# Kernel optimization log

Measured on AMD Instinct MI355X. Metric: run time of the kernel, lower is better.

Reference implementation:

```python
import jax, jax.numpy as jnp
import numpy as np

N_NODES = 100000
N_EDGES = 3200000
N_FEAT = 128
N_HID = 64


def gcn_conv(x, src, dst, ew, W, b, n):
    # x: [N, Fin]; src/dst: [E'] incl. self-loops; ew: [E'] edge weights
    xw = x @ W  # [N, Fout]
    deg = jax.ops.segment_sum(ew, dst, num_segments=n)  # [N]
    dinv = jnp.where(deg > 0, jax.lax.rsqrt(jnp.maximum(deg, 1e-12)), 0.0)
    norm = dinv[src] * ew * dinv[dst]  # [E']
    out = jax.ops.segment_sum(norm[:, None] * xw[src], dst, num_segments=n)
    return out + b


def setup_inputs() -> dict:
    key = jax.random.key(0)
    k = jax.random.split(key, 8)
    x = jax.random.normal(k[0], (N_NODES, N_FEAT), dtype=jnp.float32)
    edge_index = jax.random.randint(k[1], (2, N_EDGES), 0, N_NODES, dtype=jnp.int32)
    edge_attr = jax.random.uniform(k[2], (N_EDGES,), dtype=jnp.float32)
    s1 = 1.0 / np.sqrt(N_FEAT)
    s2 = 1.0 / np.sqrt(N_HID)
    W1 = jax.random.uniform(k[3], (N_FEAT, N_HID), minval=-s1, maxval=s1, dtype=jnp.float32)
    b1 = jnp.zeros((N_HID,), dtype=jnp.float32)
    W2 = jax.random.uniform(k[4], (N_HID, 1), minval=-s2, maxval=s2, dtype=jnp.float32)
    b2 = jnp.zeros((1,), dtype=jnp.float32)
    return {"x": x, "edge_index": edge_index, "edge_attr": edge_attr,
            "W1": W1, "b1": b1, "W2": W2, "b2": b2}


def reference(x, edge_index, edge_attr, W1, b1, W2, b2):
    n = x.shape[0]
    # add self-loops with weight 1 (PyG gcn_norm, improved=False)
    loop = jnp.arange(n, dtype=edge_index.dtype)
    src = jnp.concatenate([edge_index[0], loop])
    dst = jnp.concatenate([edge_index[1], loop])
    ew = jnp.concatenate([edge_attr, jnp.ones((n,), dtype=edge_attr.dtype)])
    h = gcn_conv(x, src, dst, ew, W1, b1, n)
    h = jax.nn.relu(h)
    # dropout is identity in eval mode
    out = gcn_conv(h, src, dst, ew, W2, b2, n)
    return out
```

## Files before the change

kernel.cpp:

```cpp
#include <hip/hip_runtime.h>
#include <hip/hip_fp16.h>


#define NPB_LOG 6
#define NPB     64
#define PCAP    2432
#define MAXPART 1600
#define NEDG    4096

typedef _Float16 f16x8 __attribute__((ext_vector_type(8)));
typedef float    f32x4 __attribute__((ext_vector_type(4)));

__global__ void k_initcur(int* __restrict__ gcur, int npart) {
    int i = blockIdx.x * blockDim.x + threadIdx.x;
    if (i < npart) gcur[i] = i * PCAP;
}

__global__ __launch_bounds__(256) void k_binA(const int* __restrict__ src,
                                              const int* __restrict__ dst,
                                              const float* __restrict__ ea,
                                              int* __restrict__ gcur,
                                              uint2* __restrict__ part,
                                              int E, int npart) {
    __shared__ int hist[MAXPART];
    __shared__ int base[MAXPART];
    int t = threadIdx.x;
    int c0 = blockIdx.x * NEDG;
    for (int i = t; i < npart; i += 256) hist[i] = 0;
    __syncthreads();
    const int ITER = NEDG / 256;
    int dv[ITER];
#pragma unroll
    for (int j = 0; j < ITER; ++j) {
        int e = c0 + j * 256 + t;
        dv[j] = (e < E) ? dst[e] : -1;
        if (dv[j] >= 0) atomicAdd(&hist[dv[j] >> NPB_LOG], 1);
    }
    __syncthreads();
    for (int i = t; i < npart; i += 256) {
        int h = hist[i];
        if (h > 0) base[i] = atomicAdd(&gcur[i], h);
        hist[i] = 0;
    }
    __syncthreads();
#pragma unroll
    for (int j = 0; j < ITER; ++j) {
        if (dv[j] >= 0) {
            int e = c0 + j * 256 + t;
            int b = dv[j] >> NPB_LOG;
            int p = base[b] + atomicAdd(&hist[b], 1);
            if (p < (b + 1) * PCAP)
                part[p] = make_uint2((uint)src[e] | ((uint)(dv[j] & (NPB - 1)) << 17),
                                     __float_as_uint(ea[e]));
        }
    }
}

__global__ __launch_bounds__(256) void k_deg(const int* __restrict__ gcur,
                                             const uint2* __restrict__ part,
                                             float* __restrict__ dinv, int n) {
    __shared__ float wsum[NPB];
    int b = blockIdx.x, t = threadIdx.x;
    if (t < NPB) wsum[t] = 0.0f;
    __syncthreads();
    int beg = b * PCAP;
    int len = gcur[b] - beg;
    if (len > PCAP) len = PCAP;
    for (int j = t; j < len; j += 256) {
        uint2 ed = part[beg + j];
        atomicAdd(&wsum[(ed.x >> 17) & (NPB - 1)], __uint_as_float(ed.y));
    }
    __syncthreads();
    int node = (b << NPB_LOG) + t;
    if (t < NPB && node < n) dinv[node] = rsqrtf(1.0f + wsum[t]);
}

#define XPAD 136
__global__ __launch_bounds__(256) void k_gemm1m(const float* __restrict__ x,
                                                const float* __restrict__ W1,
                                                const float* __restrict__ dinv,
                                                __half* __restrict__ xw2, int n) {
    __shared__ __align__(16) _Float16 xs[64 * XPAD];
    __shared__ __align__(16) _Float16 wt[64 * XPAD];
    int tid = threadIdx.x;
    int row0 = blockIdx.x * 64;
    for (int i = tid; i < 64 * 32; i += 256) {
        int r = i >> 5, k4 = i & 31;
        float4 f = make_float4(0.f, 0.f, 0.f, 0.f);
        int gr = row0 + r;
        if (gr < n) f = ((const float4*)x)[(size_t)gr * 32 + k4];
        union { _Float16 h[4]; uint2 u; } tmp;
        tmp.h[0] = (_Float16)f.x; tmp.h[1] = (_Float16)f.y;
        tmp.h[2] = (_Float16)f.z; tmp.h[3] = (_Float16)f.w;
        *(uint2*)&xs[r * XPAD + k4 * 4] = tmp.u;
    }
    for (int i = tid; i < 128 * 64; i += 256) {
        int k = i >> 6, nn = i & 63;
        wt[nn * XPAD + k] = (_Float16)W1[i];
    }
    __syncthreads();

    int strip = tid >> 6;
    int lane  = tid & 63;
    int quad  = lane >> 4;
    int m     = lane & 15;
    f32x4 acc[4] = {{0,0,0,0},{0,0,0,0},{0,0,0,0},{0,0,0,0}};
#pragma unroll
    for (int kc = 0; kc < 4; ++kc) {
        f16x8 a = *(const f16x8*)&xs[(strip * 16 + m) * XPAD + kc * 32 + quad * 8];
#pragma unroll
        for (int nt = 0; nt < 4; ++nt) {
            f16x8 b = *(const f16x8*)&wt[(nt * 16 + m) * XPAD + kc * 32 + quad * 8];
            acc[nt] = __builtin_amdgcn_mfma_f32_16x16x32_f16(a, b, acc[nt], 0, 0, 0);
        }
    }
    float dv[4];
#pragma unroll
    for (int reg = 0; reg < 4; ++reg) {
        int gr = row0 + strip * 16 + quad * 4 + reg;
        dv[reg] = (gr < n) ? dinv[gr] : 0.0f;
    }
#pragma unroll
    for (int nt = 0; nt < 4; ++nt) {
#pragma unroll
        for (int reg = 0; reg < 4; ++reg) {
            int gr = row0 + strip * 16 + quad * 4 + reg;
            if (gr < n)
                xw2[(size_t)gr * 64 + nt * 16 + m] = __float2half(dv[reg] * acc[nt][reg]);
        }
    }
}

__global__ __launch_bounds__(256) void k_aggS1(const int* __restrict__ gcur,
                                               const uint2* __restrict__ part,
                                               const float* __restrict__ dinv,
                                               const __half* __restrict__ xw2,
                                               const float* __restrict__ b1,
                                               const float* __restrict__ W2,
                                               float* __restrict__ g, int n) {
    __shared__ uint2 stag[PCAP];
    __shared__ int cnt[NPB], sbeg[NPB], cur[NPB];
    int b = blockIdx.x, t = threadIdx.x;
    int lane = t & 63, wv = t >> 6;
    if (t < NPB) cnt[t] = 0;
    __syncthreads();
    int beg = b * PCAP;
    int len = gcur[b] - beg;
    if (len > PCAP) len = PCAP;
    for (int j = t; j < len; j += 256)
        atomicAdd(&cnt[(part[beg + j].x >> 17) & (NPB - 1)], 1);
    __syncthreads();
    if (t < 64) {
        int v = cnt[t], s = v;
        for (int off = 1; off < 64; off <<= 1) {
            int u = __shfl_up(s, off, 64);
            if (t >= off) s += u;
        }
        sbeg[t] = s - v;
        cur[t]  = s - v;
    }
    __syncthreads();
    for (int j = t; j < len; j += 256) {
        uint2 ed = part[beg + j];
        int p = atomicAdd(&cur[(ed.x >> 17) & (NPB - 1)], 1);
        stag[p] = make_uint2(ed.x & 0x1FFFF, ed.y);
    }
    __syncthreads();
    float b1v = b1[lane], w2v = W2[lane];
    int nbase = b << NPB_LOG;
#pragma unroll 1
    for (int k = 0; k < 16; ++k) {
        int r = k * 4 + wv;
        int node = nbase + r;
        if (node >= n) continue;
        int s0 = sbeg[r], lr = cnt[r];
        float acc = __half2float(xw2[(size_t)node * 64 + lane]);
        for (int j0 = 0; j0 < lr; j0 += 64) {
            int idx = j0 + lane;
            int c = 0; float w = 0.0f;
            if (idx < lr) {
                uint2 ed = stag[s0 + idx];
                c = (int)ed.x;
                w = __uint_as_float(ed.y);
            }
            int m = min(64, lr - j0);
            int j = 0;
            for (; j + 8 <= m; j += 8) {
                int   c0 = __shfl(c, j,     64);
                int   c1 = __shfl(c, j + 1, 64);
                int   c2 = __shfl(c, j + 2, 64);
                int   c3 = __shfl(c, j + 3, 64);
                int   c4 = __shfl(c, j + 4, 64);
                int   c5 = __shfl(c, j + 5, 64);
                int   c6 = __shfl(c, j + 6, 64);
                int   c7 = __shfl(c, j + 7, 64);
                float w0 = __shfl(w, j,     64);
                float w1 = __shfl(w, j + 1, 64);
                float w2 = __shfl(w, j + 2, 64);
                float w3 = __shfl(w, j + 3, 64);
                float w4 = __shfl(w, j + 4, 64);
                float w5 = __shfl(w, j + 5, 64);
                float w6 = __shfl(w, j + 6, 64);
                float w7 = __shfl(w, j + 7, 64);
                float v0 = __half2float(xw2[(size_t)c0 * 64 + lane]);
                float v1 = __half2float(xw2[(size_t)c1 * 64 + lane]);
                float v2 = __half2float(xw2[(size_t)c2 * 64 + lane]);
                float v3 = __half2float(xw2[(size_t)c3 * 64 + lane]);
                float v4 = __half2float(xw2[(size_t)c4 * 64 + lane]);
                float v5 = __half2float(xw2[(size_t)c5 * 64 + lane]);
                float v6 = __half2float(xw2[(size_t)c6 * 64 + lane]);
                float v7 = __half2float(xw2[(size_t)c7 * 64 + lane]);
                acc += w0 * v0; acc += w1 * v1; acc += w2 * v2; acc += w3 * v3;
                acc += w4 * v4; acc += w5 * v5; acc += w6 * v6; acc += w7 * v7;
            }
            for (; j < m; ++j) {
                int   cj = __shfl(c, j, 64);
                float wj = __shfl(w, j, 64);
                acc += wj * __half2float(xw2[(size_t)cj * 64 + lane]);
            }
        }
        float di = dinv[node];
        float h = fmaxf(di * acc + b1v, 0.0f) * w2v;
        for (int off = 32; off; off >>= 1) h += __shfl_down(h, off, 64);
        if (lane == 0) g[node] = di * h;
    }
}

__global__ __launch_bounds__(256) void k_agg2(const int* __restrict__ gcur,
                                              const uint2* __restrict__ part,
                                              const float* __restrict__ dinv,
                                              const float* __restrict__ g,
                                              const float* __restrict__ b2,
                                              float* __restrict__ out, int n) {
    __shared__ float accs[4][NPB];
    int b = blockIdx.x, t = threadIdx.x;
    int wv = t >> 6;
    accs[t >> 6][t & 63] = 0.0f;
    __syncthreads();
    int beg = b * PCAP;
    int len = gcur[b] - beg;
    if (len > PCAP) len = PCAP;
    for (int j = t; j < len; j += 256) {
        uint2 ed = part[beg + j];
        atomicAdd(&accs[wv][(ed.x >> 17) & (NPB - 1)],
                  __uint_as_float(ed.y) * g[ed.x & 0x1FFFF]);
    }
    __syncthreads();
    if (t < NPB) {
        int node = (b << NPB_LOG) + t;
        if (node < n) {
            float p = accs[0][t] + accs[1][t] + accs[2][t] + accs[3][t];
            out[node] = b2[0] + dinv[node] * (g[node] + p);
        }
    }
}

extern "C" void kernel_launch(void* const* d_in, const int* in_sizes, int n_in,
                              void* d_out, int out_size, void* d_ws, size_t ws_size,
                              hipStream_t stream) {
    const float* x  = (const float*)d_in[0];
    const int*   ei = (const int*)  d_in[1];
    const float* ea = (const float*)d_in[2];
    const float* W1 = (const float*)d_in[3];
    const float* b1 = (const float*)d_in[4];
    const float* W2 = (const float*)d_in[5];
    const float* b2 = (const float*)d_in[6];
    float* out = (float*)d_out;

    int n = in_sizes[0] / 128;
    int E = in_sizes[1] / 2;
    const int* src = ei;
    const int* dst = ei + E;
    int npart = (n + NPB - 1) >> NPB_LOG;

    int*    ws   = (int*)d_ws;
    int*    gcur = ws;
    uint2*  part = (uint2*)(ws + MAXPART);
    size_t  psz  = (size_t)npart * PCAP;
    __half* xw2  = (__half*)(ws + MAXPART + psz * 2);
    float*  dinv = (float*)(ws + MAXPART + psz * 2 + (size_t)n * 32);
    float*  g    = dinv + n;

    k_initcur<<<(npart + 255) / 256, 256, 0, stream>>>(gcur, npart);
    k_binA  <<<(E + NEDG - 1) / NEDG, 256, 0, stream>>>(src, dst, ea, gcur, part, E, npart);
    k_deg   <<<npart, 256, 0, stream>>>(gcur, part, dinv, n);
    k_gemm1m<<<(n + 63) / 64, 256, 0, stream>>>(x, W1, dinv, xw2, n);
    k_aggS1 <<<npart, 256, 0, stream>>>(gcur, part, dinv, xw2, b1, W2, g, n);
    k_agg2  <<<npart, 256, 0, stream>>>(gcur, part, dinv, g, b2, out, n);
}
```

Before: 371.9 us.

## Aggregate layer-1 edges via shared-memory float atomics instead of per-node sorting

Result: slower. 1.470 ms (+295.3%).

```diff
diff --git a/kernel.cpp b/kernel.cpp
--- a/kernel.cpp
+++ b/kernel.cpp
@@ -131,96 +131,72 @@
     }
 }
 
-__global__ __launch_bounds__(256) void k_aggS1(const int* __restrict__ gcur,
+__global__ __launch_bounds__(256) void k_agg1L(const int* __restrict__ gcur,
                                                const uint2* __restrict__ part,
                                                const float* __restrict__ dinv,
                                                const __half* __restrict__ xw2,
                                                const float* __restrict__ b1,
                                                const float* __restrict__ W2,
                                                float* __restrict__ g, int n) {
-    __shared__ uint2 stag[PCAP];
-    __shared__ int cnt[NPB], sbeg[NPB], cur[NPB];
+    __shared__ float inner[NPB * 64];
+    __shared__ uint2 esc[4][64];
     int b = blockIdx.x, t = threadIdx.x;
     int lane = t & 63, wv = t >> 6;
-    if (t < NPB) cnt[t] = 0;
+    int nbase = b << NPB_LOG;
+    for (int r = wv; r < NPB; r += 4) {
+        int node = nbase + r;
+        inner[r * 64 + lane] = (node < n) ? __half2float(xw2[(size_t)node * 64 + lane])
+                                          : 0.0f;
+    }
     __syncthreads();
     int beg = b * PCAP;
     int len = gcur[b] - beg;
     if (len > PCAP) len = PCAP;
-    for (int j = t; j < len; j += 256)
-        atomicAdd(&cnt[(part[beg + j].x >> 17) & (NPB - 1)], 1);
-    __syncthreads();
-    if (t < 64) {
-        int v = cnt[t], s = v;
-        for (int off = 1; off < 64; off <<= 1) {
-            int u = __shfl_up(s, off, 64);
-            if (t >= off) s += u;
-        }
-        sbeg[t] = s - v;
-        cur[t]  = s - v;
-    }
-    __syncthreads();
-    for (int j = t; j < len; j += 256) {
-        uint2 ed = part[beg + j];
-        int p = atomicAdd(&cur[(ed.x >> 17) & (NPB - 1)], 1);
-        stag[p] = make_uint2(ed.x & 0x1FFFF, ed.y);
+    for (int e0 = wv * 64; e0 < len; e0 += 256) {
+        int idx = e0 + lane;
+        uint2 ed = (idx < len) ? part[beg + idx] : make_uint2(0u, 0u);
+        esc[wv][lane] = ed;
+        int m = min(64, len - e0);
+        int j = 0;
+        for (; j + 8 <= m; j += 8) {
+            uint2 e0v = esc[wv][j + 0];
+            uint2 e1v = esc[wv][j + 1];
+            uint2 e2v = esc[wv][j + 2];
+            uint2 e3v = esc[wv][j + 3];
+            uint2 e4v = esc[wv][j + 4];
+            uint2 e5v = esc[wv][j + 5];
+            uint2 e6v = esc[wv][j + 6];
+            uint2 e7v = esc[wv][j + 7];
+            float v0 = __half2float(xw2[(size_t)(e0v.x & 0x1FFFF) * 64 + lane]);
+            float v1 = __half2float(xw2[(size_t)(e1v.x & 0x1FFFF) * 64 + lane]);
+            float v2 = __half2float(xw2[(size_t)(e2v.x & 0x1FFFF) * 64 + lane]);
+            float v3 = __half2float(xw2[(size_t)(e3v.x & 0x1FFFF) * 64 + lane]);
+            float v4 = __half2float(xw2[(size_t)(e4v.x & 0x1FFFF) * 64 + lane]);
+            float v5 = __half2float(xw2[(size_t)(e5v.x & 0x1FFFF) * 64 + lane]);
+            float v6 = __half2float(xw2[(size_t)(e6v.x & 0x1FFFF) * 64 + lane]);
+            float v7 = __half2float(xw2[(size_t)(e7v.x & 0x1FFFF) * 64 + lane]);
+            atomicAdd(&inner[((e0v.x >> 17) & 63) * 64 + lane], __uint_as_float(e0v.y) * v0);
+            atomicAdd(&inner[((e1v.x >> 17) & 63) * 64 + lane], __uint_as_float(e1v.y) * v1);
+            atomicAdd(&inner[((e2v.x >> 17) & 63) * 64 + lane], __uint_as_float(e2v.y) * v2);
+            atomicAdd(&inner[((e3v.x >> 17) & 63) * 64 + lane], __uint_as_float(e3v.y) * v3);
+            atomicAdd(&inner[((e4v.x >> 17) & 63) * 64 + lane], __uint_as_float(e4v.y) * v4);
+            atomicAdd(&inner[((e5v.x >> 17) & 63) * 64 + lane], __uint_as_float(e5v.y) * v5);
+            atomicAdd(&inner[((e6v.x >> 17) & 63) * 64 + lane], __uint_as_float(e6v.y) * v6);
+            atomicAdd(&inner[((e7v.x >> 17) & 63) * 64 + lane], __uint_as_float(e7v.y) * v7);
+        }
+        for (; j < m; ++j) {
+            uint2 ev = esc[wv][j];
+            float v = __half2float(xw2[(size_t)(ev.x & 0x1FFFF) * 64 + lane]);
+            atomicAdd(&inner[((ev.x >> 17) & 63) * 64 + lane], __uint_as_float(ev.y) * v);
+        }
     }
     __syncthreads();
     float b1v = b1[lane], w2v = W2[lane];
-    int nbase = b << NPB_LOG;
-#pragma unroll 1
-    for (int k = 0; k < 16; ++k) {
-        int r = k * 4 + wv;
+    for (int r = wv; r < NPB; r += 4) {
         int node = nbase + r;
         if (node >= n) continue;
-        int s0 = sbeg[r], lr = cnt[r];
-        float acc = __half2float(xw2[(size_t)node * 64 + lane]);
-        for (int j0 = 0; j0 < lr; j0 += 64) {
-            int idx = j0 + lane;
-            int c = 0; float w = 0.0f;
-            if (idx < lr) {
-                uint2 ed = stag[s0 + idx];
-                c = (int)ed.x;
-                w = __uint_as_float(ed.y);
-            }
-            int m = min(64, lr - j0);
-            int j = 0;
-            for (; j + 8 <= m; j += 8) {
-                int   c0 = __shfl(c, j,     64);
-                int   c1 = __shfl(c, j + 1, 64);
-                int   c2 = __shfl(c, j + 2, 64);
-                int   c3 = __shfl(c, j + 3, 64);
-                int   c4 = __shfl(c, j + 4, 64);
-                int   c5 = __shfl(c, j + 5, 64);
-                int   c6 = __shfl(c, j + 6, 64);
-                int   c7 = __shfl(c, j + 7, 64);
-                float w0 = __shfl(w, j,     64);
-                float w1 = __shfl(w, j + 1, 64);
-                float w2 = __shfl(w, j + 2, 64);
-                float w3 = __shfl(w, j + 3, 64);
-                float w4 = __shfl(w, j + 4, 64);
-                float w5 = __shfl(w, j + 5, 64);
-                float w6 = __shfl(w, j + 6, 64);
-                float w7 = __shfl(w, j + 7, 64);
-                float v0 = __half2float(xw2[(size_t)c0 * 64 + lane]);
-                float v1 = __half2float(xw2[(size_t)c1 * 64 + lane]);
-                float v2 = __half2float(xw2[(size_t)c2 * 64 + lane]);
-                float v3 = __half2float(xw2[(size_t)c3 * 64 + lane]);
-                float v4 = __half2float(xw2[(size_t)c4 * 64 + lane]);
-                float v5 = __half2float(xw2[(size_t)c5 * 64 + lane]);
-                float v6 = __half2float(xw2[(size_t)c6 * 64 + lane]);
-                float v7 = __half2float(xw2[(size_t)c7 * 64 + lane]);
-                acc += w0 * v0; acc += w1 * v1; acc += w2 * v2; acc += w3 * v3;
-                acc += w4 * v4; acc += w5 * v5; acc += w6 * v6; acc += w7 * v7;
-            }
-            for (; j < m; ++j) {
-                int   cj = __shfl(c, j, 64);
-                float wj = __shfl(w, j, 64);
-                acc += wj * __half2float(xw2[(size_t)cj * 64 + lane]);
-            }
-        }
         float di = dinv[node];
-        float h = fmaxf(di * acc + b1v, 0.0f) * w2v;
+        float h = fmaxf(di * inner[r * 64 + lane] + b1v, 0.0f) * w2v;
         for (int off = 32; off; off >>= 1) h += __shfl_down(h, off, 64);
         if (lane == 0) g[node] = di * h;
     }
@@ -285,6 +261,6 @@
     k_binA  <<<(E + NEDG - 1) / NEDG, 256, 0, stream>>>(src, dst, ea, gcur, part, E, npart);
     k_deg   <<<npart, 256, 0, stream>>>(gcur, part, dinv, n);
     k_gemm1m<<<(n + 63) / 64, 256, 0, stream>>>(x, W1, dinv, xw2, n);
-    k_aggS1 <<<npart, 256, 0, stream>>>(gcur, part, dinv, xw2, b1, W2, g, n);
+    k_agg1L <<<npart, 256, 0, stream>>>(gcur, part, dinv, xw2, b1, W2, g, n);
     k_agg2  <<<npart, 256, 0, stream>>>(gcur, part, dinv, g, b2, out, n);
 }
```
